# Performance work log

Hardware: AMD Instinct MI355X
Metric: run time of the kernel (lower is better)

## Reference

```python
import jax, jax.numpy as jnp
import numpy as np

SORB = 64      # spin orbitals (sequence length)
NELE = 32      # electrons
H = 512        # num_hiddens
B = 4096       # batch
ALPHA = NELE // 2                      # = beta = 16 (spin-up / spin-down electrons)
MIN_I = min(SORB - 2 * ALPHA, 2 * ALPHA)  # = 32; symmetry mask active for i >= MIN_I
EPS = 1e-12


def setup_inputs() -> dict:
    key = jax.random.key(0)
    ks = jax.random.split(key, 10)
    s_in = 1.0 / np.sqrt(2.0)
    s_h = 1.0 / np.sqrt(H)
    return {
        "x": jax.random.randint(ks[0], (B, SORB), 0, 2, dtype=jnp.int32),  # occupancies {0,1}
        "W_ih0": jax.random.normal(ks[1], (3 * H, 2), jnp.float32) * s_in,   # GRU layer0 input weights (r,z,n)
        "W_hh0": jax.random.normal(ks[2], (3 * H, H), jnp.float32) * s_h,
        "W_ih1": jax.random.normal(ks[3], (3 * H, H), jnp.float32) * s_h,    # GRU layer1
        "W_hh1": jax.random.normal(ks[4], (3 * H, H), jnp.float32) * s_h,
        "W_amp": jax.random.normal(ks[5], (2, H), jnp.float32) * s_h,
        "b_amp": jax.random.normal(ks[6], (2,), jnp.float32) * 0.01,
        "W_phase": jax.random.normal(ks[7], (2, H), jnp.float32) * s_h,
        "b_phase": jax.random.normal(ks[8], (2,), jnp.float32) * 0.01,
    }


def _gru_cell(x_in, h, Wih, Whh):
    # PyTorch GRU (bias=False), gate order r, z, n
    gi = x_in @ Wih.T          # (B, 3H)
    gh = h @ Whh.T             # (B, 3H)
    r = jax.nn.sigmoid(gi[:, :H] + gh[:, :H])
    z = jax.nn.sigmoid(gi[:, H:2 * H] + gh[:, H:2 * H])
    n = jnp.tanh(gi[:, 2 * H:] + r * gh[:, 2 * H:])
    return (1.0 - z) * n + z * h


def reference(x, W_ih0, W_hh0, W_ih1, W_hh1, W_amp, b_amp, W_phase, b_phase):
    dt = W_ih0.dtype
    bits = x.astype(jnp.int32)           # (B, SORB) occupancies
    nb = bits.shape[0]

    def step(carry, inp):
        h0, h1, x0, amp, phase, nup, ndn = carry
        i, b_i = inp                      # site index, occupancy bits (B,)
        h0n = _gru_cell(x0, h0, W_ih0, W_hh0)
        h1n = _gru_cell(h0n, h1, W_ih1, W_hh1)
        y = h1n                           # (B, H)
        # amplitude: sqrt(softmax(linear))
        y_amp = jnp.sqrt(jax.nn.softmax(y @ W_amp.T + b_amp, axis=1))   # (B, 2)
        # phase: pi * softsign(linear)
        ph = y @ W_phase.T + b_phase
        y_ph = jnp.pi * ph / (1.0 + jnp.abs(ph))
        # particle-number symmetry mask (alpha == beta spin sectors)
        is_even = (i % 2) == 0            # even sites: spin-up, odd: spin-down
        cnt = jnp.where(is_even, nup, ndn)
        lower = (ALPHA - SORB // 2 + i // 2).astype(dt)
        occ_ok = (cnt < ALPHA).astype(dt)
        unocc_ok = (cnt > lower).astype(dt)
        mask = jnp.stack([unocc_ok, occ_ok], axis=1)
        masked = y_amp * mask
        masked = masked / jnp.sqrt(jnp.sum(masked * masked, axis=1, keepdims=True) + EPS)
        y_amp = jnp.where(i >= MIN_I, masked, y_amp)
        # accumulate conditional amplitude / phase at the sampled occupancy
        sel_a = jnp.take_along_axis(y_amp, b_i[:, None], axis=1)[:, 0]
        sel_p = jnp.take_along_axis(y_ph, b_i[:, None], axis=1)[:, 0]
        amp = amp * sel_a
        phase = phase + sel_p
        bf = b_i.astype(dt)
        nup = nup + jnp.where(is_even, bf, 0.0)
        ndn = ndn + jnp.where(is_even, 0.0, bf)
        x0n = jax.nn.one_hot(b_i, 2, dtype=dt)  # next-step GRU input
        return (h0n, h1n, x0n, amp, phase, nup, ndn), None

    init = (
        jnp.zeros((nb, H), dt), jnp.zeros((nb, H), dt), jnp.zeros((nb, 2), dt),
        jnp.ones((nb,), dt), jnp.zeros((nb,), dt), jnp.zeros((nb,), dt), jnp.zeros((nb,), dt),
    )
    xs = (jnp.arange(SORB), bits.T)       # scan over sites
    (_, _, _, amp, phase, _, _), _ = jax.lax.scan(step, init, xs)
    # complex wavefunction psi = amp * exp(1j*phase); returned as real pair (amp, phase)
    return jnp.stack([amp, phase], axis=-1)
```

## Files before the change

### kernel.cpp

```cpp
#include <hip/hip_runtime.h>
#include <hip/hip_bf16.h>

#define SORB  64
#define HID   512
#define BATCH 4096
#define N3H   1536
#define KD    512
#define BK    64
#define PI_F  3.14159265358979f

typedef _Float16 half8 __attribute__((ext_vector_type(8)));
typedef float    floatx4 __attribute__((ext_vector_type(4)));

__device__ __forceinline__ void gload16(const void* g, void* l) {
    __builtin_amdgcn_global_load_lds(
        (const __attribute__((address_space(1))) void*)g,
        (__attribute__((address_space(3))) void*)l, 16, 0, 0);
}

__device__ __forceinline__ float sigmoidf_(float x) { return 1.f / (1.f + __expf(-x)); }
__device__ __forceinline__ float tanhf_(float x) {
    x = fminf(fmaxf(x, -15.f), 15.f);
    const float e2 = __expf(2.f * x);
    return (e2 - 1.f) / (e2 + 1.f);
}

__global__ __launch_bounds__(256) void convw_kernel(
    const float* __restrict__ w0, const float* __restrict__ w1, const float* __restrict__ w2,
    _Float16* __restrict__ o0, _Float16* __restrict__ o1, _Float16* __restrict__ o2)
{
    const int i = blockIdx.x * 256 + threadIdx.x;
    if (i < N3H * KD) {
        o0[i] = (_Float16)w0[i];
        o1[i] = (_Float16)w1[i];
        o2[i] = (_Float16)w2[i];
    }
}

__global__ __launch_bounds__(256) void init_kernel(
    float* __restrict__ amp, float* __restrict__ phase,
    int* __restrict__ nup, int* __restrict__ ndn)
{
    const int i = blockIdx.x * 256 + threadIdx.x;
    if (i < BATCH) { amp[i] = 1.f; phase[i] = 0.f; nup[i] = 0; ndn[i] = 0; }
}

__global__ __launch_bounds__(256) void step1_kernel(
    const _Float16* __restrict__ h0h_c, const _Float16* __restrict__ wh0,
    const float* __restrict__ Wih0, const int* __restrict__ bits,
    _Float16* __restrict__ h0h_n, int step)
{
    const int j0 = blockIdx.x * 64;
    const int m0 = blockIdx.y * 64;

    __shared__ __align__(16) _Float16 As[64 * BK];
    __shared__ __align__(16) _Float16 Bs[192 * BK];

    const int tid  = threadIdx.x;
    const int lane = tid & 63;
    const int wid  = tid >> 6;
    const int wm   = wid >> 1, wj = wid & 1;
    const int ku   = lane >> 4;

    floatx4 acc[2][2][3];
    const floatx4 z4 = {0.f, 0.f, 0.f, 0.f};
#pragma unroll
    for (int a = 0; a < 2; ++a)
#pragma unroll
        for (int b = 0; b < 2; ++b)
#pragma unroll
            for (int g = 0; g < 3; ++g) acc[a][b][g] = z4;

    const _Float16* a_srcp[2];
#pragma unroll
    for (int k2 = 0; k2 < 2; ++k2) {
        const int p = tid + k2 * 256, row = p >> 3, c = (p & 7) ^ (row & 7);
        a_srcp[k2] = h0h_c + (size_t)(m0 + row) * KD + c * 8;
    }
    const _Float16* b_srcp[6];
#pragma unroll
    for (int k2 = 0; k2 < 6; ++k2) {
        const int p = tid + k2 * 256, row = p >> 3, c = (p & 7) ^ (row & 7);
        const int grow = (row >> 6) * HID + j0 + (row & 63);
        b_srcp[k2] = wh0 + (size_t)grow * KD + c * 8;
    }
    _Float16* a_dst[2];
#pragma unroll
    for (int k2 = 0; k2 < 2; ++k2) a_dst[k2] = As + (size_t)(k2 * 256 + wid * 64) * 8;
    _Float16* b_dst[6];
#pragma unroll
    for (int k2 = 0; k2 < 6; ++k2) b_dst[k2] = Bs + (size_t)(k2 * 256 + wid * 64) * 8;

    int aoff[2][2], boff[2][3][2];
#pragma unroll
    for (int mf = 0; mf < 2; ++mf) {
        const int r = wm * 32 + mf * 16 + (lane & 15);
#pragma unroll
        for (int kk = 0; kk < 2; ++kk)
            aoff[mf][kk] = r * BK + (((kk * 4 + ku) ^ (r & 7)) * 8);
    }
#pragma unroll
    for (int jf = 0; jf < 2; ++jf)
#pragma unroll
        for (int g = 0; g < 3; ++g) {
            const int r = g * 64 + wj * 32 + jf * 16 + (lane & 15);
#pragma unroll
            for (int kk = 0; kk < 2; ++kk)
                boff[jf][g][kk] = r * BK + (((kk * 4 + ku) ^ (r & 7)) * 8);
        }

    for (int kt = 0; kt < 8; ++kt) {
        const int k0 = kt * BK;
#pragma unroll
        for (int k2 = 0; k2 < 2; ++k2) gload16(a_srcp[k2] + k0, a_dst[k2]);
#pragma unroll
        for (int k2 = 0; k2 < 6; ++k2) gload16(b_srcp[k2] + k0, b_dst[k2]);
        __syncthreads();
#pragma unroll
        for (int kk = 0; kk < 2; ++kk) {
            half8 af[2], bf[2][3];
#pragma unroll
            for (int mf = 0; mf < 2; ++mf) af[mf] = *(const half8*)(As + aoff[mf][kk]);
#pragma unroll
            for (int jf = 0; jf < 2; ++jf)
#pragma unroll
                for (int g = 0; g < 3; ++g) bf[jf][g] = *(const half8*)(Bs + boff[jf][g][kk]);
#pragma unroll
            for (int mf = 0; mf < 2; ++mf)
#pragma unroll
                for (int jf = 0; jf < 2; ++jf)
#pragma unroll
                    for (int g = 0; g < 3; ++g)
                        acc[mf][jf][g] = __builtin_amdgcn_mfma_f32_16x16x32_f16(
                            af[mf], bf[jf][g], acc[mf][jf][g], 0, 0, 0);
        }
        __syncthreads();
    }

#pragma unroll
    for (int mf = 0; mf < 2; ++mf)
#pragma unroll
        for (int jf = 0; jf < 2; ++jf) {
            const floatx4 gr = acc[mf][jf][0];
            const floatx4 gz = acc[mf][jf][1];
            const floatx4 gn = acc[mf][jf][2];
#pragma unroll
            for (int reg = 0; reg < 4; ++reg) {
                const int m = m0 + wm * 32 + mf * 16 + (lane >> 4) * 4 + reg;
                const int j = j0 + wj * 32 + jf * 16 + (lane & 15);
                float gir = 0.f, giz = 0.f, gin = 0.f;
                if (step > 0) {
                    const int tb = bits[m * SORB + step - 1];
                    gir = Wih0[j * 2 + tb];
                    giz = Wih0[(HID + j) * 2 + tb];
                    gin = Wih0[(2 * HID + j) * 2 + tb];
                }
                const float r  = sigmoidf_(gir + gr[reg]);
                const float zz = sigmoidf_(giz + gz[reg]);
                const float n  = tanhf_(gin + r * gn[reg]);
                const size_t idx = (size_t)m * HID + j;
                const float h  = (float)h0h_c[idx];
                h0h_n[idx] = (_Float16)((1.f - zz) * n + zz * h);
            }
        }
}

__global__ __launch_bounds__(256) void step2_kernel(
    const _Float16* __restrict__ h0h_n, const _Float16* __restrict__ h1h_c,
    const _Float16* __restrict__ wi1,   const _Float16* __restrict__ wh1,
    _Float16* __restrict__ h1h_n)
{
    const int j0 = blockIdx.x * 64;
    const int m0 = blockIdx.y * 64;

    __shared__ __align__(16) _Float16 As[64 * BK];
    __shared__ __align__(16) _Float16 Bs[192 * BK];

    const int tid  = threadIdx.x;
    const int lane = tid & 63;
    const int wid  = tid >> 6;
    const int wm   = wid >> 1, wj = wid & 1;
    const int ku   = lane >> 4;

    floatx4 acc[2][2][3];
    floatx4 accn[2][2];
    const floatx4 z4 = {0.f, 0.f, 0.f, 0.f};
#pragma unroll
    for (int a = 0; a < 2; ++a)
#pragma unroll
        for (int b = 0; b < 2; ++b) {
#pragma unroll
            for (int g = 0; g < 3; ++g) acc[a][b][g] = z4;
            accn[a][b] = z4;
        }

    _Float16* a_dst[2];
#pragma unroll
    for (int k2 = 0; k2 < 2; ++k2) a_dst[k2] = As + (size_t)(k2 * 256 + wid * 64) * 8;
    _Float16* b_dst[6];
#pragma unroll
    for (int k2 = 0; k2 < 6; ++k2) b_dst[k2] = Bs + (size_t)(k2 * 256 + wid * 64) * 8;

    int aoff[2][2], boff[2][3][2];
#pragma unroll
    for (int mf = 0; mf < 2; ++mf) {
        const int r = wm * 32 + mf * 16 + (lane & 15);
#pragma unroll
        for (int kk = 0; kk < 2; ++kk)
            aoff[mf][kk] = r * BK + (((kk * 4 + ku) ^ (r & 7)) * 8);
    }
#pragma unroll
    for (int jf = 0; jf < 2; ++jf)
#pragma unroll
        for (int g = 0; g < 3; ++g) {
            const int r = g * 64 + wj * 32 + jf * 16 + (lane & 15);
#pragma unroll
            for (int kk = 0; kk < 2; ++kk)
                boff[jf][g][kk] = r * BK + (((kk * 4 + ku) ^ (r & 7)) * 8);
        }

#pragma unroll 1
    for (int half = 0; half < 2; ++half) {
        const _Float16* Aop = half ? h1h_c : h0h_n;
        const _Float16* Wop = half ? wh1  : wi1;
        const _Float16* a_srcp[2];
#pragma unroll
        for (int k2 = 0; k2 < 2; ++k2) {
            const int p = tid + k2 * 256, row = p >> 3, c = (p & 7) ^ (row & 7);
            a_srcp[k2] = Aop + (size_t)(m0 + row) * KD + c * 8;
        }
        const _Float16* b_srcp[6];
#pragma unroll
        for (int k2 = 0; k2 < 6; ++k2) {
            const int p = tid + k2 * 256, row = p >> 3, c = (p & 7) ^ (row & 7);
            const int grow = (row >> 6) * HID + j0 + (row & 63);
            b_srcp[k2] = Wop + (size_t)grow * KD + c * 8;
        }

        for (int kt = 0; kt < 8; ++kt) {
            const int k0 = kt * BK;
#pragma unroll
            for (int k2 = 0; k2 < 2; ++k2) gload16(a_srcp[k2] + k0, a_dst[k2]);
#pragma unroll
            for (int k2 = 0; k2 < 6; ++k2) gload16(b_srcp[k2] + k0, b_dst[k2]);
            __syncthreads();
#pragma unroll
            for (int kk = 0; kk < 2; ++kk) {
                half8 af[2], bf[2][3];
#pragma unroll
                for (int mf = 0; mf < 2; ++mf) af[mf] = *(const half8*)(As + aoff[mf][kk]);
#pragma unroll
                for (int jf = 0; jf < 2; ++jf)
#pragma unroll
                    for (int g = 0; g < 3; ++g) bf[jf][g] = *(const half8*)(Bs + boff[jf][g][kk]);
#pragma unroll
                for (int mf = 0; mf < 2; ++mf)
#pragma unroll
                    for (int jf = 0; jf < 2; ++jf) {
                        acc[mf][jf][0] = __builtin_amdgcn_mfma_f32_16x16x32_f16(
                            af[mf], bf[jf][0], acc[mf][jf][0], 0, 0, 0);
                        acc[mf][jf][1] = __builtin_amdgcn_mfma_f32_16x16x32_f16(
                            af[mf], bf[jf][1], acc[mf][jf][1], 0, 0, 0);
                        if (half == 0)
                            acc[mf][jf][2] = __builtin_amdgcn_mfma_f32_16x16x32_f16(
                                af[mf], bf[jf][2], acc[mf][jf][2], 0, 0, 0);
                        else
                            accn[mf][jf] = __builtin_amdgcn_mfma_f32_16x16x32_f16(
                                af[mf], bf[jf][2], accn[mf][jf], 0, 0, 0);
                    }
            }
            __syncthreads();
        }
    }

#pragma unroll
    for (int mf = 0; mf < 2; ++mf)
#pragma unroll
        for (int jf = 0; jf < 2; ++jf) {
            const floatx4 grz = acc[mf][jf][0];
            const floatx4 gzz = acc[mf][jf][1];
            const floatx4 gin = acc[mf][jf][2];
            const floatx4 ghn = accn[mf][jf];
#pragma unroll
            for (int reg = 0; reg < 4; ++reg) {
                const int m = m0 + wm * 32 + mf * 16 + (lane >> 4) * 4 + reg;
                const int j = j0 + wj * 32 + jf * 16 + (lane & 15);
                const float r  = sigmoidf_(grz[reg]);
                const float zz = sigmoidf_(gzz[reg]);
                const float n  = tanhf_(gin[reg] + r * ghn[reg]);
                const size_t idx = (size_t)m * HID + j;
                const float h  = (float)h1h_c[idx];
                h1h_n[idx] = (_Float16)((1.f - zz) * n + zz * h);
            }
        }
}

__global__ __launch_bounds__(256) void head_kernel(
    const _Float16* __restrict__ h1h_n,
    const float* __restrict__ Wamp, const float* __restrict__ bamp,
    const float* __restrict__ Wph,  const float* __restrict__ bph,
    const int* __restrict__ bits,
    float* __restrict__ amp, float* __restrict__ phase,
    int* __restrict__ nup, int* __restrict__ ndn,
    float* __restrict__ out, int step)
{
    const int lane = threadIdx.x & 63;
    const int m    = blockIdx.x * 4 + (threadIdx.x >> 6);
    const half8 hv = *(const half8*)(h1h_n + (size_t)m * HID + lane * 8);
    float d0 = 0.f, d1 = 0.f, d2 = 0.f, d3 = 0.f;
#pragma unroll
    for (int e = 0; e < 8; ++e) {
        const int j = lane * 8 + e;
        const float hn = (float)hv[e];
        d0 += hn * Wamp[j];       d1 += hn * Wamp[HID + j];
        d2 += hn * Wph[j];        d3 += hn * Wph[HID + j];
    }
#pragma unroll
    for (int off = 1; off < 64; off <<= 1) {
        d0 += __shfl_xor(d0, off); d1 += __shfl_xor(d1, off);
        d2 += __shfl_xor(d2, off); d3 += __shfl_xor(d3, off);
    }
    if (lane == 0) {
        const float a0 = d0 + bamp[0];
        const float a1 = d1 + bamp[1];
        const float mx = fmaxf(a0, a1);
        const float e0 = __expf(a0 - mx), e1 = __expf(a1 - mx);
        const float inv = 1.f / (e0 + e1);
        float ya0 = sqrtf(e0 * inv), ya1 = sqrtf(e1 * inv);
        const float p0 = d2 + bph[0];
        const float p1 = d3 + bph[1];
        const float yp0 = PI_F * p0 / (1.f + fabsf(p0));
        const float yp1 = PI_F * p1 / (1.f + fabsf(p1));
        const int even = ((step & 1) == 0);
        const int cnt = even ? nup[m] : ndn[m];
        if (step >= 32) {
            const int lower = (step >> 1) - 16;
            const float m0v = (cnt > lower) ? ya0 : 0.f;
            const float m1v = (cnt < 16) ? ya1 : 0.f;
            const float nrm = sqrtf(m0v * m0v + m1v * m1v + 1e-12f);
            ya0 = m0v / nrm; ya1 = m1v / nrm;
        }
        const int bi = bits[m * SORB + step];
        const float na = amp[m] * (bi ? ya1 : ya0);
        const float np = phase[m] + (bi ? yp1 : yp0);
        amp[m] = na; phase[m] = np;
        if (bi) { if (even) nup[m] = cnt + 1; else ndn[m] = cnt + 1; }
        if (step == SORB - 1) {
            out[m * 2 + 0] = na;
            out[m * 2 + 1] = np;
        }
    }
}

extern "C" void kernel_launch(void* const* d_in, const int* in_sizes, int n_in,
                              void* d_out, int out_size, void* d_ws, size_t ws_size,
                              hipStream_t stream) {
    const int*   bits = (const int*)d_in[0];
    const float* Wih0 = (const float*)d_in[1];
    const float* Whh0 = (const float*)d_in[2];
    const float* Wih1 = (const float*)d_in[3];
    const float* Whh1 = (const float*)d_in[4];
    const float* Wamp = (const float*)d_in[5];
    const float* bamp = (const float*)d_in[6];
    const float* Wph  = (const float*)d_in[7];
    const float* bph  = (const float*)d_in[8];
    float* out = (float*)d_out;

    char* ws = (char*)d_ws;
    size_t off = 0;
    auto alloc = [&](size_t bytes) {
        void* p = ws + off;
        off = (off + bytes + 255) & ~(size_t)255;
        return p;
    };
    _Float16* wh0 = (_Float16*)alloc((size_t)N3H * KD * 2);
    _Float16* wi1 = (_Float16*)alloc((size_t)N3H * KD * 2);
    _Float16* wh1 = (_Float16*)alloc((size_t)N3H * KD * 2);
    _Float16* h0hA = (_Float16*)alloc((size_t)BATCH * HID * 2);
    _Float16* h0hB = (_Float16*)alloc((size_t)BATCH * HID * 2);
    _Float16* h1hA = (_Float16*)alloc((size_t)BATCH * HID * 2);
    _Float16* h1hB = (_Float16*)alloc((size_t)BATCH * HID * 2);
    float*    amp   = (float*)alloc((size_t)BATCH * 4);
    float*    phase = (float*)alloc((size_t)BATCH * 4);
    int*      nup   = (int*)alloc((size_t)BATCH * 4);
    int*      ndn   = (int*)alloc((size_t)BATCH * 4);

    _Float16* h0h[2] = {h0hA, h0hB};
    _Float16* h1h[2] = {h1hA, h1hB};

    hipMemsetAsync(h0hA, 0, (size_t)BATCH * HID * 2, stream);
    hipMemsetAsync(h1hA, 0, (size_t)BATCH * HID * 2, stream);
    convw_kernel<<<(N3H * KD + 255) / 256, 256, 0, stream>>>(Whh0, Wih1, Whh1, wh0, wi1, wh1);
    init_kernel<<<BATCH / 256, 256, 0, stream>>>(amp, phase, nup, ndn);

    for (int s = 0; s < SORB; ++s) {
        const int cur = s & 1, nxt = cur ^ 1;
        step1_kernel<<<dim3(8, 64), 256, 0, stream>>>(
            h0h[cur], wh0, Wih0, bits, h0h[nxt], s);
        step2_kernel<<<dim3(8, 64), 256, 0, stream>>>(
            h0h[nxt], h1h[cur], wi1, wh1, h1h[nxt]);
        head_kernel<<<BATCH / 4, 256, 0, stream>>>(
            h1h[nxt], Wamp, bamp, Wph, bph, bits, amp, phase, nup, ndn, out, s);
    }
}
```

Measured before the change: 3.062 ms.

## Fuse previous step's head computation into step1 kernel as extra blocks

```diff
diff --git a/kernel.cpp b/kernel.cpp
--- a/kernel.cpp
+++ b/kernel.cpp
@@ -45,268 +45,16 @@
     if (i < BATCH) { amp[i] = 1.f; phase[i] = 0.f; nup[i] = 0; ndn[i] = 0; }
 }
 
-__global__ __launch_bounds__(256) void step1_kernel(
-    const _Float16* __restrict__ h0h_c, const _Float16* __restrict__ wh0,
-    const float* __restrict__ Wih0, const int* __restrict__ bits,
-    _Float16* __restrict__ h0h_n, int step)
-{
-    const int j0 = blockIdx.x * 64;
-    const int m0 = blockIdx.y * 64;
-
-    __shared__ __align__(16) _Float16 As[64 * BK];
-    __shared__ __align__(16) _Float16 Bs[192 * BK];
-
-    const int tid  = threadIdx.x;
-    const int lane = tid & 63;
-    const int wid  = tid >> 6;
-    const int wm   = wid >> 1, wj = wid & 1;
-    const int ku   = lane >> 4;
-
-    floatx4 acc[2][2][3];
-    const floatx4 z4 = {0.f, 0.f, 0.f, 0.f};
-#pragma unroll
-    for (int a = 0; a < 2; ++a)
-#pragma unroll
-        for (int b = 0; b < 2; ++b)
-#pragma unroll
-            for (int g = 0; g < 3; ++g) acc[a][b][g] = z4;
-
-    const _Float16* a_srcp[2];
-#pragma unroll
-    for (int k2 = 0; k2 < 2; ++k2) {
-        const int p = tid + k2 * 256, row = p >> 3, c = (p & 7) ^ (row & 7);
-        a_srcp[k2] = h0h_c + (size_t)(m0 + row) * KD + c * 8;
-    }
-    const _Float16* b_srcp[6];
-#pragma unroll
-    for (int k2 = 0; k2 < 6; ++k2) {
-        const int p = tid + k2 * 256, row = p >> 3, c = (p & 7) ^ (row & 7);
-        const int grow = (row >> 6) * HID + j0 + (row & 63);
-        b_srcp[k2] = wh0 + (size_t)grow * KD + c * 8;
-    }
-    _Float16* a_dst[2];
-#pragma unroll
-    for (int k2 = 0; k2 < 2; ++k2) a_dst[k2] = As + (size_t)(k2 * 256 + wid * 64) * 8;
-    _Float16* b_dst[6];
-#pragma unroll
-    for (int k2 = 0; k2 < 6; ++k2) b_dst[k2] = Bs + (size_t)(k2 * 256 + wid * 64) * 8;
-
-    int aoff[2][2], boff[2][3][2];
-#pragma unroll
-    for (int mf = 0; mf < 2; ++mf) {
-        const int r = wm * 32 + mf * 16 + (lane & 15);
-#pragma unroll
-        for (int kk = 0; kk < 2; ++kk)
-            aoff[mf][kk] = r * BK + (((kk * 4 + ku) ^ (r & 7)) * 8);
-    }
-#pragma unroll
-    for (int jf = 0; jf < 2; ++jf)
-#pragma unroll
-        for (int g = 0; g < 3; ++g) {
-            const int r = g * 64 + wj * 32 + jf * 16 + (lane & 15);
-#pragma unroll
-            for (int kk = 0; kk < 2; ++kk)
-                boff[jf][g][kk] = r * BK + (((kk * 4 + ku) ^ (r & 7)) * 8);
-        }
-
-    for (int kt = 0; kt < 8; ++kt) {
-        const int k0 = kt * BK;
-#pragma unroll
-        for (int k2 = 0; k2 < 2; ++k2) gload16(a_srcp[k2] + k0, a_dst[k2]);
-#pragma unroll
-        for (int k2 = 0; k2 < 6; ++k2) gload16(b_srcp[k2] + k0, b_dst[k2]);
-        __syncthreads();
-#pragma unroll
-        for (int kk = 0; kk < 2; ++kk) {
-            half8 af[2], bf[2][3];
-#pragma unroll
-            for (int mf = 0; mf < 2; ++mf) af[mf] = *(const half8*)(As + aoff[mf][kk]);
-#pragma unroll
-            for (int jf = 0; jf < 2; ++jf)
-#pragma unroll
-                for (int g = 0; g < 3; ++g) bf[jf][g] = *(const half8*)(Bs + boff[jf][g][kk]);
-#pragma unroll
-            for (int mf = 0; mf < 2; ++mf)
-#pragma unroll
-                for (int jf = 0; jf < 2; ++jf)
-#pragma unroll
-                    for (int g = 0; g < 3; ++g)
-                        acc[mf][jf][g] = __builtin_amdgcn_mfma_f32_16x16x32_f16(
-                            af[mf], bf[jf][g], acc[mf][jf][g], 0, 0, 0);
-        }
-        __syncthreads();
-    }
-
-#pragma unroll
-    for (int mf = 0; mf < 2; ++mf)
-#pragma unroll
-        for (int jf = 0; jf < 2; ++jf) {
-            const floatx4 gr = acc[mf][jf][0];
-            const floatx4 gz = acc[mf][jf][1];
-            const floatx4 gn = acc[mf][jf][2];
-#pragma unroll
-            for (int reg = 0; reg < 4; ++reg) {
-                const int m = m0 + wm * 32 + mf * 16 + (lane >> 4) * 4 + reg;
-                const int j = j0 + wj * 32 + jf * 16 + (lane & 15);
-                float gir = 0.f, giz = 0.f, gin = 0.f;
-                if (step > 0) {
-                    const int tb = bits[m * SORB + step - 1];
-                    gir = Wih0[j * 2 + tb];
-                    giz = Wih0[(HID + j) * 2 + tb];
-                    gin = Wih0[(2 * HID + j) * 2 + tb];
-                }
-                const float r  = sigmoidf_(gir + gr[reg]);
-                const float zz = sigmoidf_(giz + gz[reg]);
-                const float n  = tanhf_(gin + r * gn[reg]);
-                const size_t idx = (size_t)m * HID + j;
-                const float h  = (float)h0h_c[idx];
-                h0h_n[idx] = (_Float16)((1.f - zz) * n + zz * h);
-            }
-        }
-}
-
-__global__ __launch_bounds__(256) void step2_kernel(
-    const _Float16* __restrict__ h0h_n, const _Float16* __restrict__ h1h_c,
-    const _Float16* __restrict__ wi1,   const _Float16* __restrict__ wh1,
-    _Float16* __restrict__ h1h_n)
-{
-    const int j0 = blockIdx.x * 64;
-    const int m0 = blockIdx.y * 64;
-
-    __shared__ __align__(16) _Float16 As[64 * BK];
-    __shared__ __align__(16) _Float16 Bs[192 * BK];
-
-    const int tid  = threadIdx.x;
-    const int lane = tid & 63;
-    const int wid  = tid >> 6;
-    const int wm   = wid >> 1, wj = wid & 1;
-    const int ku   = lane >> 4;
-
-    floatx4 acc[2][2][3];
-    floatx4 accn[2][2];
-    const floatx4 z4 = {0.f, 0.f, 0.f, 0.f};
-#pragma unroll
-    for (int a = 0; a < 2; ++a)
-#pragma unroll
-        for (int b = 0; b < 2; ++b) {
-#pragma unroll
-            for (int g = 0; g < 3; ++g) acc[a][b][g] = z4;
-            accn[a][b] = z4;
-        }
-
-    _Float16* a_dst[2];
-#pragma unroll
-    for (int k2 = 0; k2 < 2; ++k2) a_dst[k2] = As + (size_t)(k2 * 256 + wid * 64) * 8;
-    _Float16* b_dst[6];
-#pragma unroll
-    for (int k2 = 0; k2 < 6; ++k2) b_dst[k2] = Bs + (size_t)(k2 * 256 + wid * 64) * 8;
-
-    int aoff[2][2], boff[2][3][2];
-#pragma unroll
-    for (int mf = 0; mf < 2; ++mf) {
-        const int r = wm * 32 + mf * 16 + (lane & 15);
-#pragma unroll
-        for (int kk = 0; kk < 2; ++kk)
-            aoff[mf][kk] = r * BK + (((kk * 4 + ku) ^ (r & 7)) * 8);
-    }
-#pragma unroll
-    for (int jf = 0; jf < 2; ++jf)
-#pragma unroll
-        for (int g = 0; g < 3; ++g) {
-            const int r = g * 64 + wj * 32 + jf * 16 + (lane & 15);
-#pragma unroll
-            for (int kk = 0; kk < 2; ++kk)
-                boff[jf][g][kk] = r * BK + (((kk * 4 + ku) ^ (r & 7)) * 8);
-        }
-
-#pragma unroll 1
-    for (int half = 0; half < 2; ++half) {
-        const _Float16* Aop = half ? h1h_c : h0h_n;
-        const _Float16* Wop = half ? wh1  : wi1;
-        const _Float16* a_srcp[2];
-#pragma unroll
-        for (int k2 = 0; k2 < 2; ++k2) {
-            const int p = tid + k2 * 256, row = p >> 3, c = (p & 7) ^ (row & 7);
-            a_srcp[k2] = Aop + (size_t)(m0 + row) * KD + c * 8;
-        }
-        const _Float16* b_srcp[6];
-#pragma unroll
-        for (int k2 = 0; k2 < 6; ++k2) {
-            const int p = tid + k2 * 256, row = p >> 3, c = (p & 7) ^ (row & 7);
-            const int grow = (row >> 6) * HID + j0 + (row & 63);
-            b_srcp[k2] = Wop + (size_t)grow * KD + c * 8;
-        }
-
-        for (int kt = 0; kt < 8; ++kt) {
-            const int k0 = kt * BK;
-#pragma unroll
-            for (int k2 = 0; k2 < 2; ++k2) gload16(a_srcp[k2] + k0, a_dst[k2]);
-#pragma unroll
-            for (int k2 = 0; k2 < 6; ++k2) gload16(b_srcp[k2] + k0, b_dst[k2]);
-            __syncthreads();
-#pragma unroll
-            for (int kk = 0; kk < 2; ++kk) {
-                half8 af[2], bf[2][3];
-#pragma unroll
-                for (int mf = 0; mf < 2; ++mf) af[mf] = *(const half8*)(As + aoff[mf][kk]);
-#pragma unroll
-                for (int jf = 0; jf < 2; ++jf)
-#pragma unroll
-                    for (int g = 0; g < 3; ++g) bf[jf][g] = *(const half8*)(Bs + boff[jf][g][kk]);
-#pragma unroll
-                for (int mf = 0; mf < 2; ++mf)
-#pragma unroll
-                    for (int jf = 0; jf < 2; ++jf) {
-                        acc[mf][jf][0] = __builtin_amdgcn_mfma_f32_16x16x32_f16(
-                            af[mf], bf[jf][0], acc[mf][jf][0], 0, 0, 0);
-                        acc[mf][jf][1] = __builtin_amdgcn_mfma_f32_16x16x32_f16(
-                            af[mf], bf[jf][1], acc[mf][jf][1], 0, 0, 0);
-                        if (half == 0)
-                            acc[mf][jf][2] = __builtin_amdgcn_mfma_f32_16x16x32_f16(
-                                af[mf], bf[jf][2], acc[mf][jf][2], 0, 0, 0);
-                        else
-                            accn[mf][jf] = __builtin_amdgcn_mfma_f32_16x16x32_f16(
-                                af[mf], bf[jf][2], accn[mf][jf], 0, 0, 0);
-                    }
-            }
-            __syncthreads();
-        }
-    }
-
-#pragma unroll
-    for (int mf = 0; mf < 2; ++mf)
-#pragma unroll
-        for (int jf = 0; jf < 2; ++jf) {
-            const floatx4 grz = acc[mf][jf][0];
-            const floatx4 gzz = acc[mf][jf][1];
-            const floatx4 gin = acc[mf][jf][2];
-            const floatx4 ghn = accn[mf][jf];
-#pragma unroll
-            for (int reg = 0; reg < 4; ++reg) {
-                const int m = m0 + wm * 32 + mf * 16 + (lane >> 4) * 4 + reg;
-                const int j = j0 + wj * 32 + jf * 16 + (lane & 15);
-                const float r  = sigmoidf_(grz[reg]);
-                const float zz = sigmoidf_(gzz[reg]);
-                const float n  = tanhf_(gin[reg] + r * ghn[reg]);
-                const size_t idx = (size_t)m * HID + j;
-                const float h  = (float)h1h_c[idx];
-                h1h_n[idx] = (_Float16)((1.f - zz) * n + zz * h);
-            }
-        }
-}
-
-__global__ __launch_bounds__(256) void head_kernel(
-    const _Float16* __restrict__ h1h_n,
+__device__ __forceinline__ void head_row(
+    const _Float16* __restrict__ h1, int m,
     const float* __restrict__ Wamp, const float* __restrict__ bamp,
     const float* __restrict__ Wph,  const float* __restrict__ bph,
     const int* __restrict__ bits,
     float* __restrict__ amp, float* __restrict__ phase,
     int* __restrict__ nup, int* __restrict__ ndn,
-    float* __restrict__ out, int step)
-{
-    const int lane = threadIdx.x & 63;
-    const int m    = blockIdx.x * 4 + (threadIdx.x >> 6);
-    const half8 hv = *(const half8*)(h1h_n + (size_t)m * HID + lane * 8);
+    float* __restrict__ out, int step, int lane)
+{
+    const half8 hv = *(const half8*)(h1 + (size_t)m * HID + lane * 8);
     float d0 = 0.f, d1 = 0.f, d2 = 0.f, d3 = 0.f;
 #pragma unroll
     for (int e = 0; e < 8; ++e) {
@@ -352,6 +100,288 @@
     }
 }
 
+__global__ __launch_bounds__(256) void step1_kernel(
+    const _Float16* __restrict__ h0h_c, const _Float16* __restrict__ wh0,
+    const float* __restrict__ Wih0, const int* __restrict__ bits,
+    _Float16* __restrict__ h0h_n, int step,
+    const _Float16* __restrict__ h1h_p,
+    const float* __restrict__ Wamp, const float* __restrict__ bamp,
+    const float* __restrict__ Wph,  const float* __restrict__ bph,
+    float* __restrict__ amp, float* __restrict__ phase,
+    int* __restrict__ nup, int* __restrict__ ndn, float* __restrict__ out)
+{
+    const int bid  = blockIdx.x;
+    const int tid  = threadIdx.x;
+    const int lane = tid & 63;
+    const int wid  = tid >> 6;
+
+    if (bid >= 512) {
+        if (step > 0) {
+            const int base = (bid - 512) * 32 + wid * 8;
+#pragma unroll
+            for (int rr = 0; rr < 8; ++rr)
+                head_row(h1h_p, base + rr, Wamp, bamp, Wph, bph, bits,
+                         amp, phase, nup, ndn, out, step - 1, lane);
+        }
+        return;
+    }
+
+    const int j0 = (bid & 7) * 64;
+    const int m0 = (bid >> 3) * 64;
+
+    __shared__ __align__(16) _Float16 As[64 * BK];
+    __shared__ __align__(16) _Float16 Bs[192 * BK];
+
+    const int wm = wid >> 1, wj = wid & 1;
+    const int ku = lane >> 4;
+
+    floatx4 acc[2][2][3];
+    const floatx4 z4 = {0.f, 0.f, 0.f, 0.f};
+#pragma unroll
+    for (int a = 0; a < 2; ++a)
+#pragma unroll
+        for (int b = 0; b < 2; ++b)
+#pragma unroll
+            for (int g = 0; g < 3; ++g) acc[a][b][g] = z4;
+
+    const _Float16* a_srcp[2];
+#pragma unroll
+    for (int k2 = 0; k2 < 2; ++k2) {
+        const int p = tid + k2 * 256, row = p >> 3, c = (p & 7) ^ (row & 7);
+        a_srcp[k2] = h0h_c + (size_t)(m0 + row) * KD + c * 8;
+    }
+    const _Float16* b_srcp[6];
+#pragma unroll
+    for (int k2 = 0; k2 < 6; ++k2) {
+        const int p = tid + k2 * 256, row = p >> 3, c = (p & 7) ^ (row & 7);
+        const int grow = (row >> 6) * HID + j0 + (row & 63);
+        b_srcp[k2] = wh0 + (size_t)grow * KD + c * 8;
+    }
+    _Float16* a_dst[2];
+#pragma unroll
+    for (int k2 = 0; k2 < 2; ++k2) a_dst[k2] = As + (size_t)(k2 * 256 + wid * 64) * 8;
+    _Float16* b_dst[6];
+#pragma unroll
+    for (int k2 = 0; k2 < 6; ++k2) b_dst[k2] = Bs + (size_t)(k2 * 256 + wid * 64) * 8;
+
+    int aoff[2][2], boff[2][3][2];
+#pragma unroll
+    for (int mf = 0; mf < 2; ++mf) {
+        const int r = wm * 32 + mf * 16 + (lane & 15);
+#pragma unroll
+        for (int kk = 0; kk < 2; ++kk)
+            aoff[mf][kk] = r * BK + (((kk * 4 + ku) ^ (r & 7)) * 8);
+    }
+#pragma unroll
+    for (int jf = 0; jf < 2; ++jf)
+#pragma unroll
+        for (int g = 0; g < 3; ++g) {
+            const int r = g * 64 + wj * 32 + jf * 16 + (lane & 15);
+#pragma unroll
+            for (int kk = 0; kk < 2; ++kk)
+                boff[jf][g][kk] = r * BK + (((kk * 4 + ku) ^ (r & 7)) * 8);
+        }
+
+    for (int kt = 0; kt < 8; ++kt) {
+        const int k0 = kt * BK;
+#pragma unroll
+        for (int k2 = 0; k2 < 2; ++k2) gload16(a_srcp[k2] + k0, a_dst[k2]);
+#pragma unroll
+        for (int k2 = 0; k2 < 6; ++k2) gload16(b_srcp[k2] + k0, b_dst[k2]);
+        __syncthreads();
+#pragma unroll
+        for (int kk = 0; kk < 2; ++kk) {
+            half8 af[2], bf[2][3];
+#pragma unroll
+            for (int mf = 0; mf < 2; ++mf) af[mf] = *(const half8*)(As + aoff[mf][kk]);
+#pragma unroll
+            for (int jf = 0; jf < 2; ++jf)
+#pragma unroll
+                for (int g = 0; g < 3; ++g) bf[jf][g] = *(const half8*)(Bs + boff[jf][g][kk]);
+#pragma unroll
+            for (int mf = 0; mf < 2; ++mf)
+#pragma unroll
+                for (int jf = 0; jf < 2; ++jf)
+#pragma unroll
+                    for (int g = 0; g < 3; ++g)
+                        acc[mf][jf][g] = __builtin_amdgcn_mfma_f32_16x16x32_f16(
+                            af[mf], bf[jf][g], acc[mf][jf][g], 0, 0, 0);
+        }
+        __syncthreads();
+    }
+
+#pragma unroll
+    for (int mf = 0; mf < 2; ++mf)
+#pragma unroll
+        for (int jf = 0; jf < 2; ++jf) {
+            const floatx4 gr = acc[mf][jf][0];
+            const floatx4 gz = acc[mf][jf][1];
+            const floatx4 gn = acc[mf][jf][2];
+#pragma unroll
+            for (int reg = 0; reg < 4; ++reg) {
+                const int m = m0 + wm * 32 + mf * 16 + (lane >> 4) * 4 + reg;
+                const int j = j0 + wj * 32 + jf * 16 + (lane & 15);
+                float gir = 0.f, giz = 0.f, gin = 0.f;
+                if (step > 0) {
+                    const int tb = bits[m * SORB + step - 1];
+                    gir = Wih0[j * 2 + tb];
+                    giz = Wih0[(HID + j) * 2 + tb];
+                    gin = Wih0[(2 * HID + j) * 2 + tb];
+                }
+                const float r  = sigmoidf_(gir + gr[reg]);
+                const float zz = sigmoidf_(giz + gz[reg]);
+                const float n  = tanhf_(gin + r * gn[reg]);
+                const size_t idx = (size_t)m * HID + j;
+                const float h  = (float)h0h_c[idx];
+                h0h_n[idx] = (_Float16)((1.f - zz) * n + zz * h);
+            }
+        }
+}
+
+__global__ __launch_bounds__(256) void step2_kernel(
+    const _Float16* __restrict__ h0h_n, const _Float16* __restrict__ h1h_c,
+    const _Float16* __restrict__ wi1,   const _Float16* __restrict__ wh1,
+    _Float16* __restrict__ h1h_n)
+{
+    const int j0 = blockIdx.x * 64;
+    const int m0 = blockIdx.y * 64;
+
+    __shared__ __align__(16) _Float16 As[64 * BK];
+    __shared__ __align__(16) _Float16 Bs[192 * BK];
+
+    const int tid  = threadIdx.x;
+    const int lane = tid & 63;
+    const int wid  = tid >> 6;
+    const int wm   = wid >> 1, wj = wid & 1;
+    const int ku   = lane >> 4;
+
+    floatx4 acc[2][2][3];
+    floatx4 accn[2][2];
+    const floatx4 z4 = {0.f, 0.f, 0.f, 0.f};
+#pragma unroll
+    for (int a = 0; a < 2; ++a)
+#pragma unroll
+        for (int b = 0; b < 2; ++b) {
+#pragma unroll
+            for (int g = 0; g < 3; ++g) acc[a][b][g] = z4;
+            accn[a][b] = z4;
+        }
+
+    _Float16* a_dst[2];
+#pragma unroll
+    for (int k2 = 0; k2 < 2; ++k2) a_dst[k2] = As + (size_t)(k2 * 256 + wid * 64) * 8;
+    _Float16* b_dst[6];
+#pragma unroll
+    for (int k2 = 0; k2 < 6; ++k2) b_dst[k2] = Bs + (size_t)(k2 * 256 + wid * 64) * 8;
+
+    int aoff[2][2], boff[2][3][2];
+#pragma unroll
+    for (int mf = 0; mf < 2; ++mf) {
+        const int r = wm * 32 + mf * 16 + (lane & 15);
+#pragma unroll
+        for (int kk = 0; kk < 2; ++kk)
+            aoff[mf][kk] = r * BK + (((kk * 4 + ku) ^ (r & 7)) * 8);
+    }
+#pragma unroll
+    for (int jf = 0; jf < 2; ++jf)
+#pragma unroll
+        for (int g = 0; g < 3; ++g) {
+            const int r = g * 64 + wj * 32 + jf * 16 + (lane & 15);
+#pragma unroll
+            for (int kk = 0; kk < 2; ++kk)
+                boff[jf][g][kk] = r * BK + (((kk * 4 + ku) ^ (r & 7)) * 8);
+        }
+
+#pragma unroll 1
+    for (int half = 0; half < 2; ++half) {
+        const _Float16* Aop = half ? h1h_c : h0h_n;
+        const _Float16* Wop = half ? wh1  : wi1;
+        const _Float16* a_srcp[2];
+#pragma unroll
+        for (int k2 = 0; k2 < 2; ++k2) {
+            const int p = tid + k2 * 256, row = p >> 3, c = (p & 7) ^ (row & 7);
+            a_srcp[k2] = Aop + (size_t)(m0 + row) * KD + c * 8;
+        }
+        const _Float16* b_srcp[6];
+#pragma unroll
+        for (int k2 = 0; k2 < 6; ++k2) {
+            const int p = tid + k2 * 256, row = p >> 3, c = (p & 7) ^ (row & 7);
+            const int grow = (row >> 6) * HID + j0 + (row & 63);
+            b_srcp[k2] = Wop + (size_t)grow * KD + c * 8;
+        }
+
+        for (int kt = 0; kt < 8; ++kt) {
+            const int k0 = kt * BK;
+#pragma unroll
+            for (int k2 = 0; k2 < 2; ++k2) gload16(a_srcp[k2] + k0, a_dst[k2]);
+#pragma unroll
+            for (int k2 = 0; k2 < 6; ++k2) gload16(b_srcp[k2] + k0, b_dst[k2]);
+            __syncthreads();
+#pragma unroll
+            for (int kk = 0; kk < 2; ++kk) {
+                half8 af[2], bf[2][3];
+#pragma unroll
+                for (int mf = 0; mf < 2; ++mf) af[mf] = *(const half8*)(As + aoff[mf][kk]);
+#pragma unroll
+                for (int jf = 0; jf < 2; ++jf)
+#pragma unroll
+                    for (int g = 0; g < 3; ++g) bf[jf][g] = *(const half8*)(Bs + boff[jf][g][kk]);
+#pragma unroll
+                for (int mf = 0; mf < 2; ++mf)
+#pragma unroll
+                    for (int jf = 0; jf < 2; ++jf) {
+                        acc[mf][jf][0] = __builtin_amdgcn_mfma_f32_16x16x32_f16(
+                            af[mf], bf[jf][0], acc[mf][jf][0], 0, 0, 0);
+                        acc[mf][jf][1] = __builtin_amdgcn_mfma_f32_16x16x32_f16(
+                            af[mf], bf[jf][1], acc[mf][jf][1], 0, 0, 0);
+                        if (half == 0)
+                            acc[mf][jf][2] = __builtin_amdgcn_mfma_f32_16x16x32_f16(
+                                af[mf], bf[jf][2], acc[mf][jf][2], 0, 0, 0);
+                        else
+                            accn[mf][jf] = __builtin_amdgcn_mfma_f32_16x16x32_f16(
+                                af[mf], bf[jf][2], accn[mf][jf], 0, 0, 0);
+                    }
+            }
+            __syncthreads();
+        }
+    }
+
+#pragma unroll
+    for (int mf = 0; mf < 2; ++mf)
+#pragma unroll
+        for (int jf = 0; jf < 2; ++jf) {
+            const floatx4 grz = acc[mf][jf][0];
+            const floatx4 gzz = acc[mf][jf][1];
+            const floatx4 gin = acc[mf][jf][2];
+            const floatx4 ghn = accn[mf][jf];
+#pragma unroll
+            for (int reg = 0; reg < 4; ++reg) {
+                const int m = m0 + wm * 32 + mf * 16 + (lane >> 4) * 4 + reg;
+                const int j = j0 + wj * 32 + jf * 16 + (lane & 15);
+                const float r  = sigmoidf_(grz[reg]);
+                const float zz = sigmoidf_(gzz[reg]);
+                const float n  = tanhf_(gin[reg] + r * ghn[reg]);
+                const size_t idx = (size_t)m * HID + j;
+                const float h  = (float)h1h_c[idx];
+                h1h_n[idx] = (_Float16)((1.f - zz) * n + zz * h);
+            }
+        }
+}
+
+__global__ __launch_bounds__(256) void head_kernel(
+    const _Float16* __restrict__ h1h_n,
+    const float* __restrict__ Wamp, const float* __restrict__ bamp,
+    const float* __restrict__ Wph,  const float* __restrict__ bph,
+    const int* __restrict__ bits,
+    float* __restrict__ amp, float* __restrict__ phase,
+    int* __restrict__ nup, int* __restrict__ ndn,
+    float* __restrict__ out, int step)
+{
+    const int lane = threadIdx.x & 63;
+    const int m    = blockIdx.x * 4 + (threadIdx.x >> 6);
+    head_row(h1h_n, m, Wamp, bamp, Wph, bph, bits, amp, phase, nup, ndn, out, step, lane);
+}
+
 extern "C" void kernel_launch(void* const* d_in, const int* in_sizes, int n_in,
                               void* d_out, int out_size, void* d_ws, size_t ws_size,
                               hipStream_t stream) {
@@ -395,11 +425,13 @@
 
     for (int s = 0; s < SORB; ++s) {
         const int cur = s & 1, nxt = cur ^ 1;
-        step1_kernel<<<dim3(8, 64), 256, 0, stream>>>(
-            h0h[cur], wh0, Wih0, bits, h0h[nxt], s);
+        step1_kernel<<<640, 256, 0, stream>>>(
+            h0h[cur], wh0, Wih0, bits, h0h[nxt], s,
+            h1h[cur],
+            Wamp, bamp, Wph, bph, amp, phase, nup, ndn, out);
         step2_kernel<<<dim3(8, 64), 256, 0, stream>>>(
             h0h[nxt], h1h[cur], wi1, wh1, h1h[nxt]);
-        head_kernel<<<BATCH / 4, 256, 0, stream>>>(
-            h1h[nxt], Wamp, bamp, Wph, bph, bits, amp, phase, nup, ndn, out, s);
-    }
-}
+    }
+    head_kernel<<<BATCH / 4, 256, 0, stream>>>(
+        h1h[0], Wamp, bamp, Wph, bph, bits, amp, phase, nup, ndn, out, SORB - 1);
+}
```

After: 2.827 ms. 7.7% less time.
